# Kernel tuning notes

Hardware: AMD Instinct MI355X
Metric: run time of the kernel (lower is better)

Reference implementation:

```python
import jax, jax.numpy as jnp
import numpy as np

NUM_VIEWS = 11

def setup_inputs() -> dict:
    key = jax.random.key(0)
    ks = jax.random.split(key, 6)
    BF, T, D_IN, D_OUT, R = 128, 196, 1024, 1024, 4
    B = 16
    x = jax.random.normal(ks[0], (BF, T, D_IN), dtype=jnp.float32)
    view_idx = jax.random.randint(ks[1], (B,), 0, NUM_VIEWS)
    W = jax.random.normal(ks[2], (D_OUT, D_IN), dtype=jnp.float32) * (1.0 / np.sqrt(D_IN))
    b = jax.random.normal(ks[3], (D_OUT,), dtype=jnp.float32) * 0.01
    lora_A = jax.random.normal(ks[4], (NUM_VIEWS, D_IN, R), dtype=jnp.float32) * (1.0 / np.sqrt(D_IN))
    lora_B = jax.random.normal(ks[5], (NUM_VIEWS, R, D_OUT), dtype=jnp.float32) * 0.02
    return {"x": x, "view_idx": view_idx, "W": W, "b": b, "lora_A": lora_A, "lora_B": lora_B}

def reference(x, view_idx, W, b, lora_A, lora_B):
    # base linear: [BF, T, D_in] @ [D_in, D_out]
    out = jnp.einsum('bti,oi->bto', x, W) + b
    BF = x.shape[0]
    B = view_idx.shape[0]
    if BF != B:  # static shapes -> Python branch is jit-safe
        curr = jnp.repeat(view_idx, BF // B)  # expand per-frame view index
    else:
        curr = view_idx
    curr = jnp.clip(curr, 0, NUM_VIEWS - 1)
    A = lora_A[curr]          # [BF, D_in, R] gathered per sample
    Bm = lora_B[curr]         # [BF, R, D_out]
    h = jnp.einsum('bti,bir->btr', x, A)      # low-rank projection
    lora = jnp.einsum('btr,bro->bto', h, Bm)  # back to D_out
    return out + lora
```

## Files before the change

kernel.cpp:

```cpp
#include <hip/hip_runtime.h>
#include <hip/hip_bf16.h>
#include <stdint.h>

#define M_TOT 25088
#define N_TOT 1024
#define K_TOT 1024
#define NVIEW 11
#define ROWS_PER_VIEW 1568

#define BM 128
#define BN 128
#define BK 64

typedef unsigned short u16;
typedef __bf16 bf16x8 __attribute__((ext_vector_type(8)));
typedef float f32x4 __attribute__((ext_vector_type(4)));
typedef unsigned short u16x4 __attribute__((ext_vector_type(4)));

#define XB_ELEMS ((size_t)M_TOT * K_TOT)
#define WB_ELEMS ((size_t)N_TOT * K_TOT)
#define WB_OFF_B (XB_ELEMS * 2)
#define H_OFF_B  (WB_OFF_B + WB_ELEMS * 2)
#define WS_NEEDED (H_OFF_B + (size_t)M_TOT * 4 * 4)

__device__ __forceinline__ u16 f2bf(float f) {
    union { float f; unsigned int i; } c; c.f = f;
    unsigned int i = c.i;
    return (u16)((i + 0x7FFFu + ((i >> 16) & 1u)) >> 16);
}

__global__ __launch_bounds__(256) void prep_kernel(
    const float* __restrict__ x, const float* __restrict__ W,
    const int* __restrict__ view_idx, const float* __restrict__ lora_A,
    u16* __restrict__ xb, u16* __restrict__ wb, float* __restrict__ h) {
    const int wave = threadIdx.x >> 6;
    const int lane = threadIdx.x & 63;
    const int blk  = blockIdx.x;

    if (blk >= M_TOT / 4) {
        const int row = (blk - M_TOT / 4) * 4 + wave;
        const float* src = W + (size_t)row * K_TOT;
        u16* dst = wb + (size_t)row * K_TOT;
#pragma unroll
        for (int it = 0; it < 4; ++it) {
            const int k = it * 256 + lane * 4;
            float4 v = *(const float4*)(src + k);
            u16x4 o = { f2bf(v.x), f2bf(v.y), f2bf(v.z), f2bf(v.w) };
            *(u16x4*)(dst + k) = o;
        }
        return;
    }

    const int row = blk * 4 + wave;
    int v = view_idx[row / ROWS_PER_VIEW];
    v = v < 0 ? 0 : (v > NVIEW - 1 ? NVIEW - 1 : v);
    const float* A  = lora_A + (size_t)v * (K_TOT * 4);
    const float* xr = x + (size_t)row * K_TOT;
    u16* dst = xb + (size_t)row * K_TOT;

    float a0 = 0.f, a1 = 0.f, a2 = 0.f, a3 = 0.f;
#pragma unroll
    for (int it = 0; it < 4; ++it) {
        const int k = it * 256 + lane * 4;
        float4 xv = *(const float4*)(xr + k);
        u16x4 o = { f2bf(xv.x), f2bf(xv.y), f2bf(xv.z), f2bf(xv.w) };
        *(u16x4*)(dst + k) = o;
        float4 av0 = *(const float4*)(A + (size_t)(k + 0) * 4);
        float4 av1 = *(const float4*)(A + (size_t)(k + 1) * 4);
        float4 av2 = *(const float4*)(A + (size_t)(k + 2) * 4);
        float4 av3 = *(const float4*)(A + (size_t)(k + 3) * 4);
        a0 += xv.x * av0.x + xv.y * av1.x + xv.z * av2.x + xv.w * av3.x;
        a1 += xv.x * av0.y + xv.y * av1.y + xv.z * av2.y + xv.w * av3.y;
        a2 += xv.x * av0.z + xv.y * av1.z + xv.z * av2.z + xv.w * av3.z;
        a3 += xv.x * av0.w + xv.y * av1.w + xv.z * av2.w + xv.w * av3.w;
    }
#pragma unroll
    for (int off = 32; off > 0; off >>= 1) {
        a0 += __shfl_xor(a0, off, 64);
        a1 += __shfl_xor(a1, off, 64);
        a2 += __shfl_xor(a2, off, 64);
        a3 += __shfl_xor(a3, off, 64);
    }
    if (lane == 0)
        *(float4*)(h + (size_t)row * 4) = make_float4(a0, a1, a2, a3);
}

__global__ __launch_bounds__(256) void h_only_kernel(
    const float* __restrict__ x, const int* __restrict__ view_idx,
    const float* __restrict__ lora_A, float* __restrict__ h) {
    const int row  = blockIdx.x * 4 + (threadIdx.x >> 6);
    const int lane = threadIdx.x & 63;
    int v = view_idx[row / ROWS_PER_VIEW];
    v = v < 0 ? 0 : (v > NVIEW - 1 ? NVIEW - 1 : v);
    const float* A  = lora_A + (size_t)v * (K_TOT * 4);
    const float* xr = x + (size_t)row * K_TOT;
    float a0 = 0.f, a1 = 0.f, a2 = 0.f, a3 = 0.f;
#pragma unroll
    for (int it = 0; it < 4; ++it) {
        const int k = it * 256 + lane * 4;
        float4 xv = *(const float4*)(xr + k);
        float4 av0 = *(const float4*)(A + (size_t)(k + 0) * 4);
        float4 av1 = *(const float4*)(A + (size_t)(k + 1) * 4);
        float4 av2 = *(const float4*)(A + (size_t)(k + 2) * 4);
        float4 av3 = *(const float4*)(A + (size_t)(k + 3) * 4);
        a0 += xv.x * av0.x + xv.y * av1.x + xv.z * av2.x + xv.w * av3.x;
        a1 += xv.x * av0.y + xv.y * av1.y + xv.z * av2.y + xv.w * av3.y;
        a2 += xv.x * av0.z + xv.y * av1.z + xv.z * av2.z + xv.w * av3.z;
        a3 += xv.x * av0.w + xv.y * av1.w + xv.z * av2.w + xv.w * av3.w;
    }
#pragma unroll
    for (int off = 32; off > 0; off >>= 1) {
        a0 += __shfl_xor(a0, off, 64);
        a1 += __shfl_xor(a1, off, 64);
        a2 += __shfl_xor(a2, off, 64);
        a3 += __shfl_xor(a3, off, 64);
    }
    if (lane == 0)
        *(float4*)(h + (size_t)row * 4) = make_float4(a0, a1, a2, a3);
}

template <bool CONV>
__global__ __launch_bounds__(256, 3) void gemm_lora_kernel(
    const void* __restrict__ xp, const void* __restrict__ Wp,
    const float* __restrict__ bias, const int* __restrict__ view_idx,
    const float* __restrict__ lora_B, const float* __restrict__ h,
    float* __restrict__ out) {
    __shared__ u16 As[BM * BK];
    __shared__ u16 Bs[BN * BK];

    const int tid = threadIdx.x;
    const int id = blockIdx.x;
    int bx, by;
    if (id < 1536) { const int c = id >> 6, w = id & 63; by = c * 8 + (w & 7); bx = w >> 3; }
    else           { const int r = id - 1536; by = 192 + (r & 3); bx = r >> 2; }

    const int lane = tid & 63;
    const int wave = tid >> 6;
    const int wm   = (wave >> 1) * 64;
    const int wn   = (wave & 1) * 64;
    const int l16  = lane & 15;
    const int quad = lane >> 4;
    const int sw   = l16 & 7;

    const size_t a_base = (size_t)(by * BM) * K_TOT;
    const size_t b_base = (size_t)(bx * BN) * K_TOT;

    f32x4 acc[4][4] = {};

    for (int kt = 0; kt < K_TOT / BK; ++kt) {
        const int kofs = kt * BK;
        if constexpr (!CONV) {
            const u16* x = (const u16*)xp;
            const u16* W = (const u16*)Wp;
#pragma unroll
            for (int i = 0; i < 4; ++i) {
                const int e = i * 2048 + tid * 8;
                const int r = e >> 6;
                const int c = (((tid & 7) ^ (r & 7)) << 3);
                __builtin_amdgcn_global_load_lds(
                    (const __attribute__((address_space(1))) void*)(x + a_base + (size_t)r * K_TOT + kofs + c),
                    (__attribute__((address_space(3))) void*)(As + e), 16, 0, 0);
                __builtin_amdgcn_global_load_lds(
                    (const __attribute__((address_space(1))) void*)(W + b_base + (size_t)r * K_TOT + kofs + c),
                    (__attribute__((address_space(3))) void*)(Bs + e), 16, 0, 0);
            }
        } else {
            const float* x = (const float*)xp;
            const float* W = (const float*)Wp;
#pragma unroll
            for (int i = 0; i < 8; ++i) {
                const int e = i * 1024 + tid * 4;
                const int r = e >> 6, o = e & 63;
                const int d = r * 64 + (((o >> 3) ^ (r & 7)) << 3) + (o & 7);
                float4 av = *(const float4*)(x + a_base + (size_t)r * K_TOT + kofs + o);
                float4 bv = *(const float4*)(W + b_base + (size_t)r * K_TOT + kofs + o);
                u16x4 ao = { f2bf(av.x), f2bf(av.y), f2bf(av.z), f2bf(av.w) };
                u16x4 bo = { f2bf(bv.x), f2bf(bv.y), f2bf(bv.z), f2bf(bv.w) };
                *(u16x4*)(As + d) = ao;
                *(u16x4*)(Bs + d) = bo;
            }
        }
        __syncthreads();
#pragma unroll
        for (int kk = 0; kk < 2; ++kk) {
            const int csw = (((kk * 4 + quad) ^ sw) << 3);
            bf16x8 a_frag[4], b_frag[4];
#pragma unroll
            for (int mi = 0; mi < 4; ++mi)
                a_frag[mi] = *(const bf16x8*)(const void*)(As + (wm + mi * 16 + l16) * BK + csw);
#pragma unroll
            for (int ni = 0; ni < 4; ++ni)
                b_frag[ni] = *(const bf16x8*)(const void*)(Bs + (wn + ni * 16 + l16) * BK + csw);
#pragma unroll
            for (int mi = 0; mi < 4; ++mi)
#pragma unroll
                for (int ni = 0; ni < 4; ++ni)
                    acc[mi][ni] = __builtin_amdgcn_mfma_f32_16x16x32_bf16(
                        a_frag[mi], b_frag[ni], acc[mi][ni], 0, 0, 0);
        }
        __syncthreads();
    }

    const int rowBase = by * BM + wm;
    const int colBase = bx * BN + wn;
    float biasv[4];
#pragma unroll
    for (int ni = 0; ni < 4; ++ni) biasv[ni] = bias[colBase + ni * 16 + l16];

    const int ve0 = (by * BM) / ROWS_PER_VIEW;
    const int ve1 = (by * BM + BM - 1) / ROWS_PER_VIEW;
    if (ve0 == ve1) {
        int v = view_idx[ve0];
        v = v < 0 ? 0 : (v > NVIEW - 1 ? NVIEW - 1 : v);
        const float* Bv = lora_B + (size_t)v * (4 * N_TOT);
        float Bvv[4][4];
#pragma unroll
        for (int r = 0; r < 4; ++r)
#pragma unroll
            for (int ni = 0; ni < 4; ++ni)
                Bvv[r][ni] = Bv[r * N_TOT + colBase + ni * 16 + l16];
#pragma unroll
        for (int mi = 0; mi < 4; ++mi) {
#pragma unroll
            for (int reg = 0; reg < 4; ++reg) {
                const int grow = rowBase + mi * 16 + quad * 4 + reg;
                const float4 hv = *(const float4*)(h + (size_t)grow * 4);
                float* orow = out + (size_t)grow * N_TOT;
#pragma unroll
                for (int ni = 0; ni < 4; ++ni) {
                    float lora = hv.x * Bvv[0][ni] + hv.y * Bvv[1][ni]
                               + hv.z * Bvv[2][ni] + hv.w * Bvv[3][ni];
                    orow[colBase + ni * 16 + l16] = acc[mi][ni][reg] + biasv[ni] + lora;
                }
            }
        }
    } else {
#pragma unroll
        for (int mi = 0; mi < 4; ++mi) {
#pragma unroll
            for (int reg = 0; reg < 4; ++reg) {
                const int grow = rowBase + mi * 16 + quad * 4 + reg;
                int v = view_idx[grow / ROWS_PER_VIEW];
                v = v < 0 ? 0 : (v > NVIEW - 1 ? NVIEW - 1 : v);
                const float4 hv = *(const float4*)(h + (size_t)grow * 4);
                const float* Bv = lora_B + (size_t)v * (4 * N_TOT);
                float* orow = out + (size_t)grow * N_TOT;
#pragma unroll
                for (int ni = 0; ni < 4; ++ni) {
                    const int gcol = colBase + ni * 16 + l16;
                    float lora = hv.x * Bv[gcol]
                               + hv.y * Bv[N_TOT + gcol]
                               + hv.z * Bv[2 * N_TOT + gcol]
                               + hv.w * Bv[3 * N_TOT + gcol];
                    orow[gcol] = acc[mi][ni][reg] + biasv[ni] + lora;
                }
            }
        }
    }
}

extern "C" void kernel_launch(void* const* d_in, const int* in_sizes, int n_in,
                              void* d_out, int out_size, void* d_ws, size_t ws_size,
                              hipStream_t stream) {
    const float* x        = (const float*)d_in[0];
    const int*   view_idx = (const int*)d_in[1];
    const float* W        = (const float*)d_in[2];
    const float* b        = (const float*)d_in[3];
    const float* lora_A   = (const float*)d_in[4];
    const float* lora_B   = (const float*)d_in[5];
    float* out = (float*)d_out;

    const dim3 ggrid((M_TOT / BM) * (N_TOT / BN));
    if (ws_size >= WS_NEEDED) {
        u16*   xb = (u16*)d_ws;
        u16*   wb = (u16*)((char*)d_ws + WB_OFF_B);
        float* h  = (float*)((char*)d_ws + H_OFF_B);
        hipLaunchKernelGGL(prep_kernel, dim3(M_TOT / 4 + N_TOT / 4), dim3(256), 0, stream,
                           x, W, view_idx, lora_A, xb, wb, h);
        hipLaunchKernelGGL((gemm_lora_kernel<false>), ggrid, dim3(256), 0, stream,
                           xb, wb, b, view_idx, lora_B, h, out);
    } else {
        float* h = (float*)d_ws;
        hipLaunchKernelGGL(h_only_kernel, dim3(M_TOT / 4), dim3(256), 0, stream,
                           x, view_idx, lora_A, h);
        hipLaunchKernelGGL((gemm_lora_kernel<true>), ggrid, dim3(256), 0, stream,
                           x, W, b, view_idx, lora_B, h, out);
    }
}
```

Before: 265.1 us.

## Double-buffer bf16 GEMM LDS tiles with BK=32 to overlap loads and MFMA

Splits the templated GEMM into a bf16 kernel and an fp32-convert kernel. The bf16 path now uses two LDS buffers of 32-wide K tiles with a new swizzle and prefetches the next tile via global_load_lds while the current tile feeds MFMAs. The goal is to hide global-to-LDS latency and remove one barrier per step. In exchange it runs twice as many iterations with less MFMA work per barrier, and the smaller K tile may reduce load efficiency.

```diff
diff --git a/kernel.cpp b/kernel.cpp
--- a/kernel.cpp
+++ b/kernel.cpp
@@ -10,12 +10,14 @@
 
 #define BM 128
 #define BN 128
-#define BK 64
 
 typedef unsigned short u16;
 typedef __bf16 bf16x8 __attribute__((ext_vector_type(8)));
 typedef float f32x4 __attribute__((ext_vector_type(4)));
 typedef unsigned short u16x4 __attribute__((ext_vector_type(4)));
+
+#define AS1 __attribute__((address_space(1)))
+#define AS3 __attribute__((address_space(3)))
 
 #define XB_ELEMS ((size_t)M_TOT * K_TOT)
 #define WB_ELEMS ((size_t)N_TOT * K_TOT)
@@ -119,14 +121,31 @@
         *(float4*)(h + (size_t)row * 4) = make_float4(a0, a1, a2, a3);
 }
 
-template <bool CONV>
-__global__ __launch_bounds__(256, 3) void gemm_lora_kernel(
-    const void* __restrict__ xp, const void* __restrict__ Wp,
+__device__ __forceinline__ void stage32(const u16* __restrict__ gA,
+                                        const u16* __restrict__ gB,
+                                        u16* lA, u16* lB, int kofs, int tid) {
+#pragma unroll
+    for (int i = 0; i < 2; ++i) {
+        const int e  = i * 2048 + tid * 8;
+        const int r  = e >> 5;
+        const int cc = tid & 3;
+        const int c  = ((cc ^ ((r >> 1) & 3)) << 3);
+        __builtin_amdgcn_global_load_lds(
+            (const AS1 void*)(gA + (size_t)r * K_TOT + kofs + c),
+            (AS3 void*)(lA + e), 16, 0, 0);
+        __builtin_amdgcn_global_load_lds(
+            (const AS1 void*)(gB + (size_t)r * K_TOT + kofs + c),
+            (AS3 void*)(lB + e), 16, 0, 0);
+    }
+}
+
+__global__ __launch_bounds__(256, 3) void gemm_bf16_kernel(
+    const u16* __restrict__ xb, const u16* __restrict__ wb,
     const float* __restrict__ bias, const int* __restrict__ view_idx,
     const float* __restrict__ lora_B, const float* __restrict__ h,
     float* __restrict__ out) {
-    __shared__ u16 As[BM * BK];
-    __shared__ u16 Bs[BN * BK];
+    __shared__ u16 As[2][BM * 32];
+    __shared__ u16 Bs[2][BN * 32];
 
     const int tid = threadIdx.x;
     const int id = blockIdx.x;
@@ -140,64 +159,41 @@
     const int wn   = (wave & 1) * 64;
     const int l16  = lane & 15;
     const int quad = lane >> 4;
-    const int sw   = l16 & 7;
-
-    const size_t a_base = (size_t)(by * BM) * K_TOT;
-    const size_t b_base = (size_t)(bx * BN) * K_TOT;
+    const int sw2  = (l16 >> 1) & 3;
+    const int csw  = ((quad ^ sw2) << 3);
+
+    const u16* gA = xb + (size_t)(by * BM) * K_TOT;
+    const u16* gB = wb + (size_t)(bx * BN) * K_TOT;
 
     f32x4 acc[4][4] = {};
 
-    for (int kt = 0; kt < K_TOT / BK; ++kt) {
-        const int kofs = kt * BK;
-        if constexpr (!CONV) {
-            const u16* x = (const u16*)xp;
-            const u16* W = (const u16*)Wp;
-#pragma unroll
-            for (int i = 0; i < 4; ++i) {
-                const int e = i * 2048 + tid * 8;
-                const int r = e >> 6;
-                const int c = (((tid & 7) ^ (r & 7)) << 3);
-                __builtin_amdgcn_global_load_lds(
-                    (const __attribute__((address_space(1))) void*)(x + a_base + (size_t)r * K_TOT + kofs + c),
-                    (__attribute__((address_space(3))) void*)(As + e), 16, 0, 0);
-                __builtin_amdgcn_global_load_lds(
-                    (const __attribute__((address_space(1))) void*)(W + b_base + (size_t)r * K_TOT + kofs + c),
-                    (__attribute__((address_space(3))) void*)(Bs + e), 16, 0, 0);
-            }
-        } else {
-            const float* x = (const float*)xp;
-            const float* W = (const float*)Wp;
-#pragma unroll
-            for (int i = 0; i < 8; ++i) {
-                const int e = i * 1024 + tid * 4;
-                const int r = e >> 6, o = e & 63;
-                const int d = r * 64 + (((o >> 3) ^ (r & 7)) << 3) + (o & 7);
-                float4 av = *(const float4*)(x + a_base + (size_t)r * K_TOT + kofs + o);
-                float4 bv = *(const float4*)(W + b_base + (size_t)r * K_TOT + kofs + o);
-                u16x4 ao = { f2bf(av.x), f2bf(av.y), f2bf(av.z), f2bf(av.w) };
-                u16x4 bo = { f2bf(bv.x), f2bf(bv.y), f2bf(bv.z), f2bf(bv.w) };
-                *(u16x4*)(As + d) = ao;
-                *(u16x4*)(Bs + d) = bo;
-            }
-        }
-        __syncthreads();
-#pragma unroll
-        for (int kk = 0; kk < 2; ++kk) {
-            const int csw = (((kk * 4 + quad) ^ sw) << 3);
-            bf16x8 a_frag[4], b_frag[4];
-#pragma unroll
-            for (int mi = 0; mi < 4; ++mi)
-                a_frag[mi] = *(const bf16x8*)(const void*)(As + (wm + mi * 16 + l16) * BK + csw);
+    stage32(gA, gB, &As[0][0], &Bs[0][0], 0, tid);
+    __syncthreads();
+
+    #pragma unroll 2
+    for (int kt = 0; kt < K_TOT / 32; ++kt) {
+        const int buf  = kt & 1;
+        const int nbuf = buf ^ 1;
+
+        if (kt + 1 < K_TOT / 32)
+            stage32(gA, gB, &As[nbuf][0], &Bs[nbuf][0], (kt + 1) * 32, tid);
+
+        bf16x8 a_frag[4], b_frag[4];
+#pragma unroll
+        for (int mi = 0; mi < 4; ++mi)
+            a_frag[mi] = *(const bf16x8*)(const void*)(
+                &As[buf][0] + (wm + mi * 16 + l16) * 32 + csw);
+#pragma unroll
+        for (int ni = 0; ni < 4; ++ni)
+            b_frag[ni] = *(const bf16x8*)(const void*)(
+                &Bs[buf][0] + (wn + ni * 16 + l16) * 32 + csw);
+#pragma unroll
+        for (int mi = 0; mi < 4; ++mi)
 #pragma unroll
             for (int ni = 0; ni < 4; ++ni)
-                b_frag[ni] = *(const bf16x8*)(const void*)(Bs + (wn + ni * 16 + l16) * BK + csw);
-#pragma unroll
-            for (int mi = 0; mi < 4; ++mi)
-#pragma unroll
-                for (int ni = 0; ni < 4; ++ni)
-                    acc[mi][ni] = __builtin_amdgcn_mfma_f32_16x16x32_bf16(
-                        a_frag[mi], b_frag[ni], acc[mi][ni], 0, 0, 0);
-        }
+                acc[mi][ni] = __builtin_amdgcn_mfma_f32_16x16x32_bf16(
+                    a_frag[mi], b_frag[ni], acc[mi][ni], 0, 0, 0);
+
         __syncthreads();
     }
 
@@ -254,6 +250,96 @@
                                + hv.w * Bv[3 * N_TOT + gcol];
                     orow[gcol] = acc[mi][ni][reg] + biasv[ni] + lora;
                 }
+            }
+        }
+    }
+}
+
+__global__ __launch_bounds__(256, 3) void gemm_conv_kernel(
+    const float* __restrict__ xp, const float* __restrict__ Wp,
+    const float* __restrict__ bias, const int* __restrict__ view_idx,
+    const float* __restrict__ lora_B, const float* __restrict__ h,
+    float* __restrict__ out) {
+    __shared__ u16 As[BM * 64];
+    __shared__ u16 Bs[BN * 64];
+
+    const int tid = threadIdx.x;
+    const int id = blockIdx.x;
+    int bx, by;
+    if (id < 1536) { const int c = id >> 6, w = id & 63; by = c * 8 + (w & 7); bx = w >> 3; }
+    else           { const int r = id - 1536; by = 192 + (r & 3); bx = r >> 2; }
+
+    const int lane = tid & 63;
+    const int wave = tid >> 6;
+    const int wm   = (wave >> 1) * 64;
+    const int wn   = (wave & 1) * 64;
+    const int l16  = lane & 15;
+    const int quad = lane >> 4;
+    const int sw   = l16 & 7;
+
+    const size_t a_base = (size_t)(by * BM) * K_TOT;
+    const size_t b_base = (size_t)(bx * BN) * K_TOT;
+
+    f32x4 acc[4][4] = {};
+
+    for (int kt = 0; kt < K_TOT / 64; ++kt) {
+        const int kofs = kt * 64;
+#pragma unroll
+        for (int i = 0; i < 8; ++i) {
+            const int e = i * 1024 + tid * 4;
+            const int r = e >> 6, o = e & 63;
+            const int d = r * 64 + (((o >> 3) ^ (r & 7)) << 3) + (o & 7);
+            float4 av = *(const float4*)(xp + a_base + (size_t)r * K_TOT + kofs + o);
+            float4 bv = *(const float4*)(Wp + b_base + (size_t)r * K_TOT + kofs + o);
+            u16x4 ao = { f2bf(av.x), f2bf(av.y), f2bf(av.z), f2bf(av.w) };
+            u16x4 bo = { f2bf(bv.x), f2bf(bv.y), f2bf(bv.z), f2bf(bv.w) };
+            *(u16x4*)(As + d) = ao;
+            *(u16x4*)(Bs + d) = bo;
+        }
+        __syncthreads();
+#pragma unroll
+        for (int kk = 0; kk < 2; ++kk) {
+            const int csw = (((kk * 4 + quad) ^ sw) << 3);
+            bf16x8 a_frag[4], b_frag[4];
+#pragma unroll
+            for (int mi = 0; mi < 4; ++mi)
+                a_frag[mi] = *(const bf16x8*)(const void*)(As + (wm + mi * 16 + l16) * 64 + csw);
+#pragma unroll
+            for (int ni = 0; ni < 4; ++ni)
+                b_frag[ni] = *(const bf16x8*)(const void*)(Bs + (wn + ni * 16 + l16) * 64 + csw);
+#pragma unroll
+            for (int mi = 0; mi < 4; ++mi)
+#pragma unroll
+                for (int ni = 0; ni < 4; ++ni)
+                    acc[mi][ni] = __builtin_amdgcn_mfma_f32_16x16x32_bf16(
+                        a_frag[mi], b_frag[ni], acc[mi][ni], 0, 0, 0);
+        }
+        __syncthreads();
+    }
+
+    const int rowBase = by * BM + wm;
+    const int colBase = bx * BN + wn;
+    float biasv[4];
+#pragma unroll
+    for (int ni = 0; ni < 4; ++ni) biasv[ni] = bias[colBase + ni * 16 + l16];
+#pragma unroll
+    for (int mi = 0; mi < 4; ++mi) {
+#pragma unroll
+        for (int reg = 0; reg < 4; ++reg) {
+            const int grow = rowBase + mi * 16 + quad * 4 + reg;
+            int v = view_idx[grow / ROWS_PER_VIEW];
+            v = v < 0 ? 0 : (v > NVIEW - 1 ? NVIEW - 1 : v);
+            const float4 hv = *(const float4*)(h + (size_t)grow * 4);
+            const float* Bv = lora_B + (size_t)v * (4 * N_TOT);
+            float* orow = out + (size_t)grow * N_TOT;
+#pragma unroll
+            for (int ni = 0; ni < 4; ++ni) {
+                const int gcol = colBase + ni * 16 + l16;
+                float lora = hv.x * Bv[gcol]
+                           + hv.y * Bv[N_TOT + gcol]
+                           + hv.z * Bv[2 * N_TOT + gcol]
+                           + hv.w * Bv[3 * N_TOT + gcol];
+                orow[gcol] = acc[mi][ni][reg] + biasv[ni] + lora;
             }
         }
     }
@@ -277,13 +363,13 @@
         float* h  = (float*)((char*)d_ws + H_OFF_B);
         hipLaunchKernelGGL(prep_kernel, dim3(M_TOT / 4 + N_TOT / 4), dim3(256), 0, stream,
                            x, W, view_idx, lora_A, xb, wb, h);
-        hipLaunchKernelGGL((gemm_lora_kernel<false>), ggrid, dim3(256), 0, stream,
+        hipLaunchKernelGGL(gemm_bf16_kernel, ggrid, dim3(256), 0, stream,
                            xb, wb, b, view_idx, lora_B, h, out);
     } else {
         float* h = (float*)d_ws;
         hipLaunchKernelGGL(h_only_kernel, dim3(M_TOT / 4), dim3(256), 0, stream,
                            x, view_idx, lora_A, h);
-        hipLaunchKernelGGL((gemm_lora_kernel<true>), ggrid, dim3(256), 0, stream,
+        hipLaunchKernelGGL(gemm_conv_kernel, ggrid, dim3(256), 0, stream,
                            x, W, b, view_idx, lora_B, h, out);
     }
 }
```

Measured after the change: 270.9 us. +2.2%, slower.
